# Kernel optimization log

Measured on AMD Instinct MI355X. Metric: run time of the kernel, lower is better.

The kernel has to match this reference:

```python
import jax, jax.numpy as jnp
import numpy as np

T, B, NI = 100, 2048, 3
NU = 128          # nh_lstm
NB = 256          # nh_bottleneck
NPC, NHD = 256, 12
INIT = NPC + NHD  # 268


def setup_inputs() -> dict:
    key = jax.random.key(0)
    ks = jax.random.split(key, 20)
    s_in = 1.0 / np.sqrt(NI)
    s_u = 1.0 / np.sqrt(NU)
    s_b = 1.0 / np.sqrt(NB)
    s_e = 1.0 / np.sqrt(INIT)
    return {
        "x": jax.random.normal(ks[0], (T, B, NI), jnp.float32),
        "init_pc": jax.random.normal(ks[1], (B, NPC), jnp.float32),
        "init_hd": jax.random.normal(ks[2], (B, NHD), jnp.float32),
        "Wz": jax.random.normal(ks[3], (NI, NU), jnp.float32) * s_in,
        "Wr": jax.random.normal(ks[4], (NI, NU), jnp.float32) * s_in,
        "Wh": jax.random.normal(ks[5], (NI, NU), jnp.float32) * s_in,
        "Uz": jax.random.normal(ks[6], (NU, NU), jnp.float32) * s_u,
        "Ur": jax.random.normal(ks[7], (NU, NU), jnp.float32) * s_u,
        "Uh": jax.random.normal(ks[8], (NU, NU), jnp.float32) * s_u,
        "bz": jnp.zeros((NU,), jnp.float32),
        "br": jnp.zeros((NU,), jnp.float32),
        "bh": jnp.zeros((NU,), jnp.float32),
        "W_embed": jax.random.normal(ks[9], (INIT, NU), jnp.float32) * s_e,
        "b_embed": jnp.zeros((NU,), jnp.float32),
        "W_bneck": jax.random.normal(ks[10], (NU, NB), jnp.float32) * s_u,  # no bias
        "W_pc": jax.random.normal(ks[11], (NB, NPC), jnp.float32) * s_b,
        "b_pc": jnp.zeros((NPC,), jnp.float32),
        "W_hd": jax.random.normal(ks[12], (NB, NHD), jnp.float32) * s_b,
        "b_hd": jnp.zeros((NHD,), jnp.float32),
    }


def reference(x, init_pc, init_hd, Wz, Wr, Wh, Uz, Ur, Uh, bz, br, bh,
              W_embed, b_embed, W_bneck, W_pc, b_pc, W_hd, b_hd):
    # state_embed(cat(initial_conds))
    init = jnp.concatenate([init_pc, init_hd], axis=1)      # [B, 268]
    h0 = init @ W_embed + b_embed                           # [B, NU]

    # hoist input projections out of the recurrence: [T, B, NU]
    xz = x @ Wz + bz
    xr = x @ Wr + br
    xh = x @ Wh + bh

    def step(h, xs):
        xz_t, xr_t, xh_t = xs
        z = jax.nn.sigmoid(xz_t + h @ Uz)
        r = jax.nn.sigmoid(xr_t + h @ Ur)
        h_tw = jnp.tanh(xh_t + (r * h) @ Uh)
        h = (1.0 - z) * h + z * h_tw
        return h, h

    final_state, states = jax.lax.scan(step, h0, (xz, xr, xh))  # states: [T, B, NU]

    # bottleneck (dropout in eval mode = identity) and logit heads, batched over T
    bottleneck = states @ W_bneck                           # [T, B, NB]
    logits_pc = bottleneck @ W_pc + b_pc                    # [T, B, NPC]
    logits_hd = bottleneck @ W_hd + b_hd                    # [T, B, NHD]
    return logits_hd, logits_pc, bottleneck, states, final_state
```

## Files before the change

### kernel.cpp

```cpp
#include <hip/hip_runtime.h>

#define TT 100
#define BB 2048
#define NI 3
#define NU 128
#define NB 256
#define NPC 256
#define NHD 12

typedef __attribute__((ext_vector_type(8))) short short8;
typedef __attribute__((ext_vector_type(4))) float f32x4;

__device__ __forceinline__ float fast_sigmoid(float x) {
  return 1.0f / (1.0f + __expf(-x));
}
__device__ __forceinline__ float fast_tanh(float x) {
  return 1.0f - 2.0f / (__expf(2.0f * x) + 1.0f);
}
__device__ __forceinline__ short f2bf(float f) {
  uint32_t u = __float_as_uint(f);
  u += 0x7FFF + ((u >> 16) & 1);
  return (short)(u >> 16);
}
__device__ __forceinline__ float bf2f(short s) {
  return __uint_as_float(((uint32_t)(uint16_t)s) << 16);
}
__device__ __forceinline__ void lds_barrier() {
  asm volatile("s_waitcnt lgkmcnt(0)" ::: "memory");
  __builtin_amdgcn_s_barrier();
}

__global__ __launch_bounds__(256) void embed_kernel(
    const float* __restrict__ init_pc, const float* __restrict__ init_hd,
    const float* __restrict__ W_embed, const float* __restrict__ b_embed,
    float* __restrict__ h0) {
  __shared__ float pcs[2][NPC];
  __shared__ float hds[2][NHD];
  const int tid = threadIdx.x;
  const int b0 = blockIdx.x * 2;

  for (int idx = tid; idx < 2 * NPC; idx += 256)
    pcs[idx >> 8][idx & 255] =
        init_pc[(size_t)(b0 + (idx >> 8)) * NPC + (idx & 255)];
  if (tid < 2 * NHD) {
    int rr = tid / NHD, cc = tid - rr * NHD;
    hds[rr][cc] = init_hd[(size_t)(b0 + rr) * NHD + cc];
  }
  __syncthreads();

  const int half = tid >> 7;
  const int j = tid & 127;
  const float* Wp = W_embed + j;
  float a0 = 0.f, a1 = 0.f, a2 = 0.f, a3 = 0.f;
#pragma unroll 4
  for (int k = 0; k < NPC; k += 4) {
    a0 = fmaf(pcs[half][k + 0], Wp[(k + 0) * NU], a0);
    a1 = fmaf(pcs[half][k + 1], Wp[(k + 1) * NU], a1);
    a2 = fmaf(pcs[half][k + 2], Wp[(k + 2) * NU], a2);
    a3 = fmaf(pcs[half][k + 3], Wp[(k + 3) * NU], a3);
  }
#pragma unroll
  for (int k = 0; k < NHD; ++k)
    a0 = fmaf(hds[half][k], Wp[(NPC + k) * NU], a0);
  float acc = b_embed[j] + ((a0 + a1) + (a2 + a3));
  h0[(size_t)(b0 + half) * NU + j] = acc;
}

__global__ __launch_bounds__(512, 2) void gru_mfma_kernel(
    const float* __restrict__ x, const float* __restrict__ h0,
    const float* __restrict__ Wz, const float* __restrict__ Wr,
    const float* __restrict__ Wh, const float* __restrict__ Uz,
    const float* __restrict__ Ur, const float* __restrict__ Uh,
    const float* __restrict__ bz, const float* __restrict__ br,
    const float* __restrict__ bh, float* __restrict__ states,
    float* __restrict__ final_state) {
  __shared__ short h_hi[16 * 128];
  __shared__ short h_lo[16 * 128];
  __shared__ short p_hi[16 * 128];
  __shared__ short p_lo[16 * 128];
  __shared__ float xs[TT][8][4];

  const int tid = threadIdx.x;
  const int lane = tid & 63;
  const int w = tid >> 6;
  const int ln15 = lane & 15;
  const int g4 = lane >> 4;
  const int col = w * 16 + ln15;
  const int row0 = blockIdx.x * 8;

  for (int idx = tid; idx < TT * 32; idx += 512) {
    const int t = idx >> 5, rem = idx & 31, r = rem >> 2, i = rem & 3;
    xs[t][r][i] = (i < 3) ? x[(size_t)(t * BB + row0 + r) * NI + i] : 0.0f;
  }

  const float wz0 = Wz[col], wz1 = Wz[NU + col], wz2 = Wz[2 * NU + col];
  const float wr0 = Wr[col], wr1 = Wr[NU + col], wr2 = Wr[2 * NU + col];
  const float wh0 = Wh[col], wh1 = Wh[NU + col], wh2 = Wh[2 * NU + col];
  const float bzv = bz[col], brv = br[col], bhv = bh[col];

  short8 Uzh[4], Uzl[4], Urh[4], Url[4], Uhh[4], Uhl[4];
#pragma unroll
  for (int kt = 0; kt < 4; ++kt) {
#pragma unroll
    for (int e = 0; e < 8; ++e) {
      const int kk = kt * 32 + g4 * 8 + e;
      float v;
      short hi;
      v = Uz[kk * NU + col];
      hi = f2bf(v);
      Uzh[kt][e] = hi;
      Uzl[kt][e] = f2bf(v - bf2f(hi));
      v = Ur[kk * NU + col];
      hi = f2bf(v);
      Urh[kt][e] = hi;
      Url[kt][e] = f2bf(v - bf2f(hi));
      v = Uh[kk * NU + col];
      hi = f2bf(v);
      Uhh[kt][e] = hi;
      Uhl[kt][e] = f2bf(v - bf2f(hi));
    }
  }

  float hreg[4];
#pragma unroll
  for (int q = 0; q < 4; ++q) {
    const int row = g4 * 4 + q;
    hreg[q] = (row < 8) ? h0[(size_t)(row0 + row) * NU + col] : 0.0f;
    const int off = row * 256 + ((col * 2) ^ ((row & 7) << 4));
    const short hi = f2bf(hreg[q]);
    *(short*)((char*)h_hi + off) = hi;
    *(short*)((char*)h_lo + off) = f2bf(hreg[q] - bf2f(hi));
  }
  __syncthreads();

  int foff[4];
#pragma unroll
  for (int kt = 0; kt < 4; ++kt)
    foff[kt] = ln15 * 256 + ((kt * 64 + g4 * 16) ^ ((ln15 & 7) << 4));
  int woff[4];
#pragma unroll
  for (int q = 0; q < 4; ++q) {
    const int row = g4 * 4 + q;
    woff[q] = row * 256 + ((col * 2) ^ ((row & 7) << 4));
  }

  for (int t = 0; t < TT; ++t) {
    short8 ahi[4], alo[4];
#pragma unroll
    for (int kt = 0; kt < 4; ++kt) {
      ahi[kt] = *(const short8*)((const char*)h_hi + foff[kt]);
      alo[kt] = *(const short8*)((const char*)h_lo + foff[kt]);
    }
    float4 xrow[4];
#pragma unroll
    for (int q = 0; q < 4; ++q)
      xrow[q] = *(const float4*)xs[t][(g4 * 4 + q) & 7];

    f32x4 r0, r1 = {0.f, 0.f, 0.f, 0.f};
#pragma unroll
    for (int q = 0; q < 4; ++q)
      r0[q] =
          fmaf(xrow[q].x, wr0, fmaf(xrow[q].y, wr1, fmaf(xrow[q].z, wr2, brv)));
    r0 = __builtin_amdgcn_mfma_f32_16x16x32_bf16(ahi[0], Urh[0], r0, 0, 0, 0);
    r1 = __builtin_amdgcn_mfma_f32_16x16x32_bf16(ahi[1], Urh[1], r1, 0, 0, 0);
    r0 = __builtin_amdgcn_mfma_f32_16x16x32_bf16(alo[0], Urh[0], r0, 0, 0, 0);
    r1 = __builtin_amdgcn_mfma_f32_16x16x32_bf16(alo[1], Urh[1], r1, 0, 0, 0);
    r0 = __builtin_amdgcn_mfma_f32_16x16x32_bf16(ahi[0], Url[0], r0, 0, 0, 0);
    r1 = __builtin_amdgcn_mfma_f32_16x16x32_bf16(ahi[1], Url[1], r1, 0, 0, 0);
    r0 = __builtin_amdgcn_mfma_f32_16x16x32_bf16(ahi[2], Urh[2], r0, 0, 0, 0);
    r1 = __builtin_amdgcn_mfma_f32_16x16x32_bf16(ahi[3], Urh[3], r1, 0, 0, 0);
    r0 = __builtin_amdgcn_mfma_f32_16x16x32_bf16(alo[2], Urh[2], r0, 0, 0, 0);
    r1 = __builtin_amdgcn_mfma_f32_16x16x32_bf16(alo[3], Urh[3], r1, 0, 0, 0);
    r0 = __builtin_amdgcn_mfma_f32_16x16x32_bf16(ahi[2], Url[2], r0, 0, 0, 0);
    r1 = __builtin_amdgcn_mfma_f32_16x16x32_bf16(ahi[3], Url[3], r1, 0, 0, 0);

    if (g4 < 2) {
#pragma unroll
      for (int q = 0; q < 4; ++q) {
        const float rh = fast_sigmoid(r0[q] + r1[q]) * hreg[q];
        const short hi = f2bf(rh);
        *(short*)((char*)p_hi + woff[q]) = hi;
        *(short*)((char*)p_lo + woff[q]) = f2bf(rh - bf2f(hi));
      }
    }
    lds_barrier();

    short8 phi[4], plo[4];
#pragma unroll
    for (int kt = 0; kt < 4; ++kt) {
      phi[kt] = *(const short8*)((const char*)p_hi + foff[kt]);
      plo[kt] = *(const short8*)((const char*)p_lo + foff[kt]);
    }
    f32x4 z0, z1 = {0.f, 0.f, 0.f, 0.f};
    f32x4 hh0, hh1 = {0.f, 0.f, 0.f, 0.f};
#pragma unroll
    for (int q = 0; q < 4; ++q) {
      z0[q] =
          fmaf(xrow[q].x, wz0, fmaf(xrow[q].y, wz1, fmaf(xrow[q].z, wz2, bzv)));
      hh0[q] =
          fmaf(xrow[q].x, wh0, fmaf(xrow[q].y, wh1, fmaf(xrow[q].z, wh2, bhv)));
    }
    z0 = __builtin_amdgcn_mfma_f32_16x16x32_bf16(ahi[0], Uzh[0], z0, 0, 0, 0);
    z1 = __builtin_amdgcn_mfma_f32_16x16x32_bf16(ahi[1], Uzh[1], z1, 0, 0, 0);
    hh0 = __builtin_amdgcn_mfma_f32_16x16x32_bf16(phi[0], Uhh[0], hh0, 0, 0, 0);
    hh1 = __builtin_amdgcn_mfma_f32_16x16x32_bf16(phi[1], Uhh[1], hh1, 0, 0, 0);
    z0 = __builtin_amdgcn_mfma_f32_16x16x32_bf16(alo[0], Uzh[0], z0, 0, 0, 0);
    z1 = __builtin_amdgcn_mfma_f32_16x16x32_bf16(alo[1], Uzh[1], z1, 0, 0, 0);
    hh0 = __builtin_amdgcn_mfma_f32_16x16x32_bf16(plo[0], Uhh[0], hh0, 0, 0, 0);
    hh1 = __builtin_amdgcn_mfma_f32_16x16x32_bf16(plo[1], Uhh[1], hh1, 0, 0, 0);
    z0 = __builtin_amdgcn_mfma_f32_16x16x32_bf16(ahi[0], Uzl[0], z0, 0, 0, 0);
    z1 = __builtin_amdgcn_mfma_f32_16x16x32_bf16(ahi[1], Uzl[1], z1, 0, 0, 0);
    hh0 = __builtin_amdgcn_mfma_f32_16x16x32_bf16(phi[0], Uhl[0], hh0, 0, 0, 0);
    hh1 = __builtin_amdgcn_mfma_f32_16x16x32_bf16(phi[1], Uhl[1], hh1, 0, 0, 0);
    z0 = __builtin_amdgcn_mfma_f32_16x16x32_bf16(ahi[2], Uzh[2], z0, 0, 0, 0);
    z1 = __builtin_amdgcn_mfma_f32_16x16x32_bf16(ahi[3], Uzh[3], z1, 0, 0, 0);
    hh0 = __builtin_amdgcn_mfma_f32_16x16x32_bf16(phi[2], Uhh[2], hh0, 0, 0, 0);
    hh1 = __builtin_amdgcn_mfma_f32_16x16x32_bf16(phi[3], Uhh[3], hh1, 0, 0, 0);
    z0 = __builtin_amdgcn_mfma_f32_16x16x32_bf16(alo[2], Uzh[2], z0, 0, 0, 0);
    z1 = __builtin_amdgcn_mfma_f32_16x16x32_bf16(alo[3], Uzh[3], z1, 0, 0, 0);
    hh0 = __builtin_amdgcn_mfma_f32_16x16x32_bf16(plo[2], Uhh[2], hh0, 0, 0, 0);
    hh1 = __builtin_amdgcn_mfma_f32_16x16x32_bf16(plo[3], Uhh[3], hh1, 0, 0, 0);
    z0 = __builtin_amdgcn_mfma_f32_16x16x32_bf16(ahi[2], Uzl[2], z0, 0, 0, 0);
    z1 = __builtin_amdgcn_mfma_f32_16x16x32_bf16(ahi[3], Uzl[3], z1, 0, 0, 0);
    hh0 = __builtin_amdgcn_mfma_f32_16x16x32_bf16(phi[2], Uhl[2], hh0, 0, 0, 0);
    hh1 = __builtin_amdgcn_mfma_f32_16x16x32_bf16(phi[3], Uhl[3], hh1, 0, 0, 0);

#pragma unroll
    for (int q = 0; q < 4; ++q) {
      const float zg = fast_sigmoid(z0[q] + z1[q]);
      const float htw = fast_tanh(hh0[q] + hh1[q]);
      hreg[q] = fmaf(zg, htw - hreg[q], hreg[q]);
    }
    if (g4 < 2) {
#pragma unroll
      for (int q = 0; q < 4; ++q) {
        const short hi = f2bf(hreg[q]);
        *(short*)((char*)h_hi + woff[q]) = hi;
        *(short*)((char*)h_lo + woff[q]) = f2bf(hreg[q] - bf2f(hi));
      }
    }
    lds_barrier();
    if (g4 < 2) {
#pragma unroll
      for (int q = 0; q < 4; ++q)
        states[((size_t)t * BB + row0 + g4 * 4 + q) * NU + col] = hreg[q];
    }
  }

  if (g4 < 2) {
#pragma unroll
    for (int q = 0; q < 4; ++q)
      final_state[(size_t)(row0 + g4 * 4 + q) * NU + col] = hreg[q];
  }
}

__global__ __launch_bounds__(256) void prepack_kernel(
    const float* __restrict__ Wb, const float* __restrict__ Wpc,
    const float* __restrict__ Whd, short* __restrict__ Wb_pack,
    short* __restrict__ Wpc_pack, short* __restrict__ Whd_pack) {
  int t = blockIdx.x * 256 + threadIdx.x;
  if (t >= 200 * 64) return;
  int fb = t >> 6, lane = t & 63;
  const float* W;
  short* out;
  int n_tile, k_tile, N, local;
  if (fb < 64) {
    W = Wb; out = Wb_pack; local = fb; n_tile = fb >> 2; k_tile = fb & 3; N = 256;
  } else if (fb < 192) {
    int f = fb - 64;
    W = Wpc; out = Wpc_pack; local = f; n_tile = f >> 3; k_tile = f & 7; N = 256;
  } else {
    int f = fb - 192;
    W = Whd; out = Whd_pack; local = f; n_tile = 0; k_tile = f; N = 12;
  }
  short8 p;
#pragma unroll
  for (int e = 0; e < 8; ++e) {
    int k = k_tile * 32 + (lane >> 4) * 8 + e;
    int colc = n_tile * 16 + (lane & 15);
    float v = (colc < N) ? W[k * N + colc] : 0.0f;
    p[e] = f2bf(v);
  }
  *((short8*)out + (local * 64 + lane)) = p;
}

__global__ __launch_bounds__(256, 3) void heads_mfma_kernel(
    const float* __restrict__ states, const short* __restrict__ Wb_pack,
    const short* __restrict__ Wpc_pack, const short* __restrict__ Whd_pack,
    const float* __restrict__ b_pc, const float* __restrict__ b_hd,
    float* __restrict__ out_hd, float* __restrict__ out_pc,
    float* __restrict__ out_bn) {
  __shared__ short s_lds[64 * 128];
  __shared__ short bn_lds[64 * 256];
  const int tid = threadIdx.x;
  const size_t R0 = (size_t)blockIdx.x * 64;

  for (int c = tid; c < 1024; c += 256) {
    int row = c >> 4, s16 = c & 15;
    const float* src = states + (R0 + row) * 128 + s16 * 8;
    float4 v0 = *(const float4*)src;
    float4 v1 = *(const float4*)(src + 4);
    short8 p;
    p[0] = f2bf(v0.x); p[1] = f2bf(v0.y); p[2] = f2bf(v0.z); p[3] = f2bf(v0.w);
    p[4] = f2bf(v1.x); p[5] = f2bf(v1.y); p[6] = f2bf(v1.z); p[7] = f2bf(v1.w);
    int byte = row * 256 + ((s16 * 16) ^ ((row & 7) << 4));
    *(short8*)((char*)s_lds + byte) = p;
  }
  __syncthreads();

  const int lane = tid & 63;
  const int wave = tid >> 6;
  const int ln15 = lane & 15;
  const int ln4 = lane >> 4;
  const int r0 = wave * 16;

  {
    short8 a[4];
#pragma unroll
    for (int kt = 0; kt < 4; ++kt) {
      int byte =
          (r0 + ln15) * 256 + ((kt * 64 + ln4 * 16) ^ ((ln15 & 7) << 4));
      a[kt] = *(const short8*)((const char*)s_lds + byte);
    }
#pragma unroll
    for (int nt = 0; nt < 16; ++nt) {
      f32x4 acc = {0.f, 0.f, 0.f, 0.f};
      const short8* bp = (const short8*)Wb_pack + (nt * 4) * 64 + lane;
#pragma unroll
      for (int kt = 0; kt < 4; ++kt)
        acc = __builtin_amdgcn_mfma_f32_16x16x32_bf16(a[kt], bp[kt * 64], acc,
                                                      0, 0, 0);
      int colc = nt * 16 + ln15;
#pragma unroll
      for (int q = 0; q < 4; ++q) {
        int row = r0 + ln4 * 4 + q;
        out_bn[(R0 + row) * NB + colc] = acc[q];
        int byte = row * 512 + ((colc * 2) ^ ((row & 7) << 4));
        *(short*)((char*)bn_lds + byte) = f2bf(acc[q]);
      }
    }
  }
  __syncthreads();

  {
    short8 ab[8];
#pragma unroll
    for (int kt = 0; kt < 8; ++kt) {
      int byte =
          (r0 + ln15) * 512 + ((kt * 64 + ln4 * 16) ^ ((ln15 & 7) << 4));
      ab[kt] = *(const short8*)((const char*)bn_lds + byte);
    }
#pragma unroll
    for (int nt = 0; nt < 16; ++nt) {
      int colc = nt * 16 + ln15;
      float bias = b_pc[colc];
      f32x4 acc = {bias, bias, bias, bias};
      const short8* bp = (const short8*)Wpc_pack + (nt * 8) * 64 + lane;
#pragma unroll
      for (int kt = 0; kt < 8; ++kt)
        acc = __builtin_amdgcn_mfma_f32_16x16x32_bf16(ab[kt], bp[kt * 64], acc,
                                                      0, 0, 0);
#pragma unroll
      for (int q = 0; q < 4; ++q)
        out_pc[(R0 + r0 + ln4 * 4 + q) * NPC + colc] = acc[q];
    }
    {
      int colc = ln15;
      float bias = (colc < NHD) ? b_hd[colc] : 0.0f;
      f32x4 acc = {bias, bias, bias, bias};
      const short8* bp = (const short8*)Whd_pack + lane;
#pragma unroll
      for (int kt = 0; kt < 8; ++kt)
        acc = __builtin_amdgcn_mfma_f32_16x16x32_bf16(ab[kt], bp[kt * 64], acc,
                                                      0, 0, 0);
      if (colc < NHD) {
#pragma unroll
        for (int q = 0; q < 4; ++q)
          out_hd[(R0 + r0 + ln4 * 4 + q) * NHD + colc] = acc[q];
      }
    }
  }
}

extern "C" void kernel_launch(void* const* d_in, const int* in_sizes, int n_in,
                              void* d_out, int out_size, void* d_ws,
                              size_t ws_size, hipStream_t stream) {
  (void)in_sizes;
  (void)n_in;
  (void)out_size;
  (void)ws_size;
  const float* x = (const float*)d_in[0];
  const float* init_pc = (const float*)d_in[1];
  const float* init_hd = (const float*)d_in[2];
  const float* Wz = (const float*)d_in[3];
  const float* Wr = (const float*)d_in[4];
  const float* Wh = (const float*)d_in[5];
  const float* Uz = (const float*)d_in[6];
  const float* Ur = (const float*)d_in[7];
  const float* Uh = (const float*)d_in[8];
  const float* bz = (const float*)d_in[9];
  const float* br = (const float*)d_in[10];
  const float* bh = (const float*)d_in[11];
  const float* W_embed = (const float*)d_in[12];
  const float* b_embed = (const float*)d_in[13];
  const float* W_bneck = (const float*)d_in[14];
  const float* W_pc = (const float*)d_in[15];
  const float* b_pc = (const float*)d_in[16];
  const float* W_hd = (const float*)d_in[17];
  const float* b_hd = (const float*)d_in[18];

  float* out = (float*)d_out;
  float* out_hd = out;
  float* out_pc = out_hd + (size_t)TT * BB * NHD;
  float* out_bn = out_pc + (size_t)TT * BB * NPC;
  float* out_st = out_bn + (size_t)TT * BB * NB;
  float* out_fs = out_st + (size_t)TT * BB * NU;

  float* h0 = (float*)d_ws;
  short* Wb_pack = (short*)((char*)d_ws + (1 << 20));
  short* Wpc_pack = Wb_pack + 64 * 64 * 8;
  short* Whd_pack = Wpc_pack + 128 * 64 * 8;

  prepack_kernel<<<50, 256, 0, stream>>>(W_bneck, W_pc, W_hd, Wb_pack,
                                         Wpc_pack, Whd_pack);
  embed_kernel<<<BB / 2, 256, 0, stream>>>(init_pc, init_hd, W_embed, b_embed,
                                           h0);
  gru_mfma_kernel<<<BB / 8, 512, 0, stream>>>(x, h0, Wz, Wr, Wh, Uz, Ur, Uh,
                                              bz, br, bh, out_st, out_fs);
  heads_mfma_kernel<<<(TT * BB) / 64, 256, 0, stream>>>(
      out_st, Wb_pack, Wpc_pack, Whd_pack, b_pc, b_hd, out_hd, out_pc, out_bn);
}
```

Measured before the change: 382.1 us.

## Halve GRU block to 4 waves each computing two column tiles

```diff
diff --git a/kernel.cpp b/kernel.cpp
--- a/kernel.cpp
+++ b/kernel.cpp
@@ -66,7 +66,7 @@
   h0[(size_t)(b0 + half) * NU + j] = acc;
 }
 
-__global__ __launch_bounds__(512, 2) void gru_mfma_kernel(
+__global__ __launch_bounds__(256, 1) void gru_mfma_kernel(
     const float* __restrict__ x, const float* __restrict__ h0,
     const float* __restrict__ Wz, const float* __restrict__ Wr,
     const float* __restrict__ Wh, const float* __restrict__ Uz,
@@ -85,64 +85,83 @@
   const int w = tid >> 6;
   const int ln15 = lane & 15;
   const int g4 = lane >> 4;
-  const int col = w * 16 + ln15;
   const int row0 = blockIdx.x * 8;
 
-  for (int idx = tid; idx < TT * 32; idx += 512) {
+  int col[2];
+  col[0] = w * 32 + ln15;
+  col[1] = w * 32 + 16 + ln15;
+
+  for (int idx = tid; idx < TT * 32; idx += 256) {
     const int t = idx >> 5, rem = idx & 31, r = rem >> 2, i = rem & 3;
     xs[t][r][i] = (i < 3) ? x[(size_t)(t * BB + row0 + r) * NI + i] : 0.0f;
   }
 
-  const float wz0 = Wz[col], wz1 = Wz[NU + col], wz2 = Wz[2 * NU + col];
-  const float wr0 = Wr[col], wr1 = Wr[NU + col], wr2 = Wr[2 * NU + col];
-  const float wh0 = Wh[col], wh1 = Wh[NU + col], wh2 = Wh[2 * NU + col];
-  const float bzv = bz[col], brv = br[col], bhv = bh[col];
-
-  short8 Uzh[4], Uzl[4], Urh[4], Url[4], Uhh[4], Uhl[4];
-#pragma unroll
-  for (int kt = 0; kt < 4; ++kt) {
-#pragma unroll
-    for (int e = 0; e < 8; ++e) {
-      const int kk = kt * 32 + g4 * 8 + e;
-      float v;
-      short hi;
-      v = Uz[kk * NU + col];
-      hi = f2bf(v);
-      Uzh[kt][e] = hi;
-      Uzl[kt][e] = f2bf(v - bf2f(hi));
-      v = Ur[kk * NU + col];
-      hi = f2bf(v);
-      Urh[kt][e] = hi;
-      Url[kt][e] = f2bf(v - bf2f(hi));
-      v = Uh[kk * NU + col];
-      hi = f2bf(v);
-      Uhh[kt][e] = hi;
-      Uhl[kt][e] = f2bf(v - bf2f(hi));
-    }
-  }
-
-  float hreg[4];
-#pragma unroll
-  for (int q = 0; q < 4; ++q) {
-    const int row = g4 * 4 + q;
-    hreg[q] = (row < 8) ? h0[(size_t)(row0 + row) * NU + col] : 0.0f;
-    const int off = row * 256 + ((col * 2) ^ ((row & 7) << 4));
-    const short hi = f2bf(hreg[q]);
-    *(short*)((char*)h_hi + off) = hi;
-    *(short*)((char*)h_lo + off) = f2bf(hreg[q] - bf2f(hi));
-  }
-  __syncthreads();
+  float wzc[2][3], wrc[2][3], whc[2][3], bzv[2], brv[2], bhv[2];
+#pragma unroll
+  for (int tau = 0; tau < 2; ++tau) {
+#pragma unroll
+    for (int i = 0; i < 3; ++i) {
+      wzc[tau][i] = Wz[i * NU + col[tau]];
+      wrc[tau][i] = Wr[i * NU + col[tau]];
+      whc[tau][i] = Wh[i * NU + col[tau]];
+    }
+    bzv[tau] = bz[col[tau]];
+    brv[tau] = br[col[tau]];
+    bhv[tau] = bh[col[tau]];
+  }
+
+  short8 Uzh[2][4], Uzl[2][4], Urh[2][4], Url[2][4], Uhh[2][4], Uhl[2][4];
+#pragma unroll
+  for (int tau = 0; tau < 2; ++tau) {
+#pragma unroll
+    for (int kt = 0; kt < 4; ++kt) {
+#pragma unroll
+      for (int e = 0; e < 8; ++e) {
+        const int kk = kt * 32 + g4 * 8 + e;
+        float v;
+        short hi;
+        v = Uz[kk * NU + col[tau]];
+        hi = f2bf(v);
+        Uzh[tau][kt][e] = hi;
+        Uzl[tau][kt][e] = f2bf(v - bf2f(hi));
+        v = Ur[kk * NU + col[tau]];
+        hi = f2bf(v);
+        Urh[tau][kt][e] = hi;
+        Url[tau][kt][e] = f2bf(v - bf2f(hi));
+        v = Uh[kk * NU + col[tau]];
+        hi = f2bf(v);
+        Uhh[tau][kt][e] = hi;
+        Uhl[tau][kt][e] = f2bf(v - bf2f(hi));
+      }
+    }
+  }
 
   int foff[4];
 #pragma unroll
   for (int kt = 0; kt < 4; ++kt)
     foff[kt] = ln15 * 256 + ((kt * 64 + g4 * 16) ^ ((ln15 & 7) << 4));
-  int woff[4];
-#pragma unroll
-  for (int q = 0; q < 4; ++q) {
-    const int row = g4 * 4 + q;
-    woff[q] = row * 256 + ((col * 2) ^ ((row & 7) << 4));
-  }
+  int woff[2][4];
+#pragma unroll
+  for (int tau = 0; tau < 2; ++tau)
+#pragma unroll
+    for (int q = 0; q < 4; ++q) {
+      const int row = g4 * 4 + q;
+      woff[tau][q] = row * 256 + ((col[tau] * 2) ^ ((row & 7) << 4));
+    }
+
+  float hreg[2][4];
+#pragma unroll
+  for (int tau = 0; tau < 2; ++tau)
+#pragma unroll
+    for (int q = 0; q < 4; ++q) {
+      const int row = g4 * 4 + q;
+      hreg[tau][q] =
+          (row < 8) ? h0[(size_t)(row0 + row) * NU + col[tau]] : 0.0f;
+      const short hi = f2bf(hreg[tau][q]);
+      *(short*)((char*)h_hi + woff[tau][q]) = hi;
+      *(short*)((char*)h_lo + woff[tau][q]) = f2bf(hreg[tau][q] - bf2f(hi));
+    }
+  __syncthreads();
 
   for (int t = 0; t < TT; ++t) {
     short8 ahi[4], alo[4];
@@ -156,32 +175,43 @@
     for (int q = 0; q < 4; ++q)
       xrow[q] = *(const float4*)xs[t][(g4 * 4 + q) & 7];
 
-    f32x4 r0, r1 = {0.f, 0.f, 0.f, 0.f};
-#pragma unroll
-    for (int q = 0; q < 4; ++q)
-      r0[q] =
-          fmaf(xrow[q].x, wr0, fmaf(xrow[q].y, wr1, fmaf(xrow[q].z, wr2, brv)));
-    r0 = __builtin_amdgcn_mfma_f32_16x16x32_bf16(ahi[0], Urh[0], r0, 0, 0, 0);
-    r1 = __builtin_amdgcn_mfma_f32_16x16x32_bf16(ahi[1], Urh[1], r1, 0, 0, 0);
-    r0 = __builtin_amdgcn_mfma_f32_16x16x32_bf16(alo[0], Urh[0], r0, 0, 0, 0);
-    r1 = __builtin_amdgcn_mfma_f32_16x16x32_bf16(alo[1], Urh[1], r1, 0, 0, 0);
-    r0 = __builtin_amdgcn_mfma_f32_16x16x32_bf16(ahi[0], Url[0], r0, 0, 0, 0);
-    r1 = __builtin_amdgcn_mfma_f32_16x16x32_bf16(ahi[1], Url[1], r1, 0, 0, 0);
-    r0 = __builtin_amdgcn_mfma_f32_16x16x32_bf16(ahi[2], Urh[2], r0, 0, 0, 0);
-    r1 = __builtin_amdgcn_mfma_f32_16x16x32_bf16(ahi[3], Urh[3], r1, 0, 0, 0);
-    r0 = __builtin_amdgcn_mfma_f32_16x16x32_bf16(alo[2], Urh[2], r0, 0, 0, 0);
-    r1 = __builtin_amdgcn_mfma_f32_16x16x32_bf16(alo[3], Urh[3], r1, 0, 0, 0);
-    r0 = __builtin_amdgcn_mfma_f32_16x16x32_bf16(ahi[2], Url[2], r0, 0, 0, 0);
-    r1 = __builtin_amdgcn_mfma_f32_16x16x32_bf16(ahi[3], Url[3], r1, 0, 0, 0);
+    f32x4 r[2][2];
+#pragma unroll
+    for (int tau = 0; tau < 2; ++tau)
+#pragma unroll
+      for (int q = 0; q < 4; ++q) {
+        r[tau][0][q] = fmaf(
+            xrow[q].x, wrc[tau][0],
+            fmaf(xrow[q].y, wrc[tau][1], fmaf(xrow[q].z, wrc[tau][2], brv[tau])));
+        r[tau][1][q] = 0.0f;
+      }
+#pragma unroll
+    for (int kp = 0; kp < 2; ++kp)
+#pragma unroll
+      for (int term = 0; term < 3; ++term)
+#pragma unroll
+        for (int kk = 0; kk < 2; ++kk) {
+          const int kt = 2 * kp + kk;
+#pragma unroll
+          for (int tau = 0; tau < 2; ++tau) {
+            const short8 A = (term == 1) ? alo[kt] : ahi[kt];
+            const short8 Bf = (term == 2) ? Url[tau][kt] : Urh[tau][kt];
+            r[tau][kk] =
+                __builtin_amdgcn_mfma_f32_16x16x32_bf16(A, Bf, r[tau][kk], 0, 0, 0);
+          }
+        }
 
     if (g4 < 2) {
 #pragma unroll
-      for (int q = 0; q < 4; ++q) {
-        const float rh = fast_sigmoid(r0[q] + r1[q]) * hreg[q];
-        const short hi = f2bf(rh);
-        *(short*)((char*)p_hi + woff[q]) = hi;
-        *(short*)((char*)p_lo + woff[q]) = f2bf(rh - bf2f(hi));
-      }
+      for (int tau = 0; tau < 2; ++tau)
+#pragma unroll
+        for (int q = 0; q < 4; ++q) {
+          const float rh =
+              fast_sigmoid(r[tau][0][q] + r[tau][1][q]) * hreg[tau][q];
+          const short hi = f2bf(rh);
+          *(short*)((char*)p_hi + woff[tau][q]) = hi;
+          *(short*)((char*)p_lo + woff[tau][q]) = f2bf(rh - bf2f(hi));
+        }
     }
     lds_barrier();
 
@@ -191,66 +221,74 @@
       phi[kt] = *(const short8*)((const char*)p_hi + foff[kt]);
       plo[kt] = *(const short8*)((const char*)p_lo + foff[kt]);
     }
-    f32x4 z0, z1 = {0.f, 0.f, 0.f, 0.f};
-    f32x4 hh0, hh1 = {0.f, 0.f, 0.f, 0.f};
-#pragma unroll
-    for (int q = 0; q < 4; ++q) {
-      z0[q] =
-          fmaf(xrow[q].x, wz0, fmaf(xrow[q].y, wz1, fmaf(xrow[q].z, wz2, bzv)));
-      hh0[q] =
-          fmaf(xrow[q].x, wh0, fmaf(xrow[q].y, wh1, fmaf(xrow[q].z, wh2, bhv)));
-    }
-    z0 = __builtin_amdgcn_mfma_f32_16x16x32_bf16(ahi[0], Uzh[0], z0, 0, 0, 0);
-    z1 = __builtin_amdgcn_mfma_f32_16x16x32_bf16(ahi[1], Uzh[1], z1, 0, 0, 0);
-    hh0 = __builtin_amdgcn_mfma_f32_16x16x32_bf16(phi[0], Uhh[0], hh0, 0, 0, 0);
-    hh1 = __builtin_amdgcn_mfma_f32_16x16x32_bf16(phi[1], Uhh[1], hh1, 0, 0, 0);
-    z0 = __builtin_amdgcn_mfma_f32_16x16x32_bf16(alo[0], Uzh[0], z0, 0, 0, 0);
-    z1 = __builtin_amdgcn_mfma_f32_16x16x32_bf16(alo[1], Uzh[1], z1, 0, 0, 0);
-    hh0 = __builtin_amdgcn_mfma_f32_16x16x32_bf16(plo[0], Uhh[0], hh0, 0, 0, 0);
-    hh1 = __builtin_amdgcn_mfma_f32_16x16x32_bf16(plo[1], Uhh[1], hh1, 0, 0, 0);
-    z0 = __builtin_amdgcn_mfma_f32_16x16x32_bf16(ahi[0], Uzl[0], z0, 0, 0, 0);
-    z1 = __builtin_amdgcn_mfma_f32_16x16x32_bf16(ahi[1], Uzl[1], z1, 0, 0, 0);
-    hh0 = __builtin_amdgcn_mfma_f32_16x16x32_bf16(phi[0], Uhl[0], hh0, 0, 0, 0);
-    hh1 = __builtin_amdgcn_mfma_f32_16x16x32_bf16(phi[1], Uhl[1], hh1, 0, 0, 0);
-    z0 = __builtin_amdgcn_mfma_f32_16x16x32_bf16(ahi[2], Uzh[2], z0, 0, 0, 0);
-    z1 = __builtin_amdgcn_mfma_f32_16x16x32_bf16(ahi[3], Uzh[3], z1, 0, 0, 0);
-    hh0 = __builtin_amdgcn_mfma_f32_16x16x32_bf16(phi[2], Uhh[2], hh0, 0, 0, 0);
-    hh1 = __builtin_amdgcn_mfma_f32_16x16x32_bf16(phi[3], Uhh[3], hh1, 0, 0, 0);
-    z0 = __builtin_amdgcn_mfma_f32_16x16x32_bf16(alo[2], Uzh[2], z0, 0, 0, 0);
-    z1 = __builtin_amdgcn_mfma_f32_16x16x32_bf16(alo[3], Uzh[3], z1, 0, 0, 0);
-    hh0 = __builtin_amdgcn_mfma_f32_16x16x32_bf16(plo[2], Uhh[2], hh0, 0, 0, 0);
-    hh1 = __builtin_amdgcn_mfma_f32_16x16x32_bf16(plo[3], Uhh[3], hh1, 0, 0, 0);
-    z0 = __builtin_amdgcn_mfma_f32_16x16x32_bf16(ahi[2], Uzl[2], z0, 0, 0, 0);
-    z1 = __builtin_amdgcn_mfma_f32_16x16x32_bf16(ahi[3], Uzl[3], z1, 0, 0, 0);
-    hh0 = __builtin_amdgcn_mfma_f32_16x16x32_bf16(phi[2], Uhl[2], hh0, 0, 0, 0);
-    hh1 = __builtin_amdgcn_mfma_f32_16x16x32_bf16(phi[3], Uhl[3], hh1, 0, 0, 0);
-
-#pragma unroll
-    for (int q = 0; q < 4; ++q) {
-      const float zg = fast_sigmoid(z0[q] + z1[q]);
-      const float htw = fast_tanh(hh0[q] + hh1[q]);
-      hreg[q] = fmaf(zg, htw - hreg[q], hreg[q]);
-    }
+    f32x4 zc[2], hc[2];
+#pragma unroll
+    for (int tau = 0; tau < 2; ++tau)
+#pragma unroll
+      for (int q = 0; q < 4; ++q) {
+        zc[tau][q] = fmaf(
+            xrow[q].x, wzc[tau][0],
+            fmaf(xrow[q].y, wzc[tau][1], fmaf(xrow[q].z, wzc[tau][2], bzv[tau])));
+        hc[tau][q] = fmaf(
+            xrow[q].x, whc[tau][0],
+            fmaf(xrow[q].y, whc[tau][1], fmaf(xrow[q].z, whc[tau][2], bhv[tau])));
+      }
+#pragma unroll
+    for (int kt = 0; kt < 4; ++kt)
+#pragma unroll
+      for (int term = 0; term < 3; ++term) {
+#pragma unroll
+        for (int tau = 0; tau < 2; ++tau) {
+          const short8 A = (term == 1) ? alo[kt] : ahi[kt];
+          const short8 Bf = (term == 2) ? Uzl[tau][kt] : Uzh[tau][kt];
+          zc[tau] =
+              __builtin_amdgcn_mfma_f32_16x16x32_bf16(A, Bf, zc[tau], 0, 0, 0);
+        }
+#pragma unroll
+        for (int tau = 0; tau < 2; ++tau) {
+          const short8 A = (term == 1) ? plo[kt] : phi[kt];
+          const short8 Bf = (term == 2) ? Uhl[tau][kt] : Uhh[tau][kt];
+          hc[tau] =
+              __builtin_amdgcn_mfma_f32_16x16x32_bf16(A, Bf, hc[tau], 0, 0, 0);
+        }
+      }
+
+#pragma unroll
+    for (int tau = 0; tau < 2; ++tau)
+#pragma unroll
+      for (int q = 0; q < 4; ++q) {
+        const float zg = fast_sigmoid(zc[tau][q]);
+        const float htw = fast_tanh(hc[tau][q]);
+        hreg[tau][q] = fmaf(zg, htw - hreg[tau][q], hreg[tau][q]);
+      }
     if (g4 < 2) {
 #pragma unroll
-      for (int q = 0; q < 4; ++q) {
-        const short hi = f2bf(hreg[q]);
-        *(short*)((char*)h_hi + woff[q]) = hi;
-        *(short*)((char*)h_lo + woff[q]) = f2bf(hreg[q] - bf2f(hi));
-      }
+      for (int tau = 0; tau < 2; ++tau)
+#pragma unroll
+        for (int q = 0; q < 4; ++q) {
+          const short hi = f2bf(hreg[tau][q]);
+          *(short*)((char*)h_hi + woff[tau][q]) = hi;
+          *(short*)((char*)h_lo + woff[tau][q]) = f2bf(hreg[tau][q] - bf2f(hi));
+        }
     }
     lds_barrier();
     if (g4 < 2) {
 #pragma unroll
+      for (int tau = 0; tau < 2; ++tau)
+#pragma unroll
+        for (int q = 0; q < 4; ++q)
+          states[((size_t)t * BB + row0 + g4 * 4 + q) * NU + col[tau]] =
+              hreg[tau][q];
+    }
+  }
+
+  if (g4 < 2) {
+#pragma unroll
+    for (int tau = 0; tau < 2; ++tau)
+#pragma unroll
       for (int q = 0; q < 4; ++q)
-        states[((size_t)t * BB + row0 + g4 * 4 + q) * NU + col] = hreg[q];
-    }
-  }
-
-  if (g4 < 2) {
-#pragma unroll
-    for (int q = 0; q < 4; ++q)
-      final_state[(size_t)(row0 + g4 * 4 + q) * NU + col] = hreg[q];
+        final_state[(size_t)(row0 + g4 * 4 + q) * NU + col[tau]] =
+            hreg[tau][q];
   }
 }
 
@@ -425,7 +463,7 @@
                                          Wpc_pack, Whd_pack);
   embed_kernel<<<BB / 2, 256, 0, stream>>>(init_pc, init_hd, W_embed, b_embed,
                                            h0);
-  gru_mfma_kernel<<<BB / 8, 512, 0, stream>>>(x, h0, Wz, Wr, Wh, Uz, Ur, Uh,
+  gru_mfma_kernel<<<BB / 8, 256, 0, stream>>>(x, h0, Wz, Wr, Wh, Uz, Ur, Uh,
                                               bz, br, bh, out_st, out_fs);
   heads_mfma_kernel<<<(TT * BB) / 64, 256, 0, stream>>>(
       out_st, Wb_pack, Wpc_pack, Whd_pack, b_pc, b_hd, out_hd, out_pc, out_bn);
```

Result: slower. 431.7 us (+13.0%).
